# Optimization experiments

Hardware: AMD Instinct MI355X
Metric: run time of the kernel (lower is better)

The kernel has to match this reference:

```python
import jax, jax.numpy as jnp
import numpy as np

H = 512
N = 512
BSZ = 8
L = 4096
DIRECTION = 2  # 0=forward, 1=backward, 2=bidirectional (split N in half)


def setup_inputs() -> dict:
    key = jax.random.key(0)
    k = jax.random.split(key, 6)
    u = jax.random.normal(k[0], (BSZ, L, H), jnp.float32)
    # variable lengths in [L//2, L]
    lengths = jax.random.randint(k[1], (BSZ,), L // 2, L + 1).astype(jnp.int32)
    # LRU init: r_min=0, r_max=1, max_phase=2*pi
    u1 = jax.random.uniform(k[2], (N,), jnp.float32)
    nu_log = jnp.log(-0.5 * jnp.log(u1))
    u2 = jax.random.uniform(k[3], (N,), jnp.float32)
    theta_log = jnp.log(2.0 * np.pi * u2)
    lam = jnp.exp(-jnp.exp(nu_log) + 1j * jnp.exp(theta_log))  # (N,) complex
    gamma = jnp.sqrt(1.0 - jnp.abs(lam) ** 2)[:, None]          # (N,1)
    B = jax.random.normal(k[4], (H, N, 2), jnp.float32) / np.float32(np.sqrt(2 * H)) * gamma
    C = jax.random.normal(k[5], (2, H, N), jnp.float32) / np.float32(np.sqrt(N))
    return {"u": u, "lengths": lengths, "nu_log": nu_log, "theta_log": theta_log, "B": B, "C": C}


def _lru_scan(lam, Bu, reverse):
    """Diagonal linear recurrence x_t = lam * x_{t-1} + Bu_t along axis 2 via associative scan.
    lam: (n,) complex; Bu: (B, n, L) complex."""
    a = jnp.broadcast_to(lam[None, :, None], Bu.shape)

    def op(e1, e2):
        a1, b1 = e1
        a2, b2 = e2
        return a1 * a2, a2 * b1 + b2

    _, x = jax.lax.associative_scan(op, (a, Bu), axis=2, reverse=reverse)
    return x


def reference(u, lengths, nu_log, theta_log, B, C):
    lam = jnp.exp(-jnp.exp(nu_log) + 1j * jnp.exp(theta_log))  # (N,)
    Bc = B[..., 0] + 1j * B[..., 1]                            # (H, N) complex
    Bu = jnp.einsum('blh,hn->bnl', u, Bc)                      # (B, N, L) complex
    mask = jnp.arange(L)[None, :] < lengths[:, None]           # (B, L)
    Bu = Bu * mask[:, None, :]
    if DIRECTION == 2:
        h = N // 2
        x = jnp.concatenate([
            _lru_scan(lam[:h], Bu[:, :h], reverse=False),
            _lru_scan(lam[h:], Bu[:, h:], reverse=True),
        ], axis=1)
    elif DIRECTION == 0:
        x = _lru_scan(lam, Bu, reverse=False)
    else:
        x = _lru_scan(lam, Bu, reverse=True)
    x = x * mask[:, None, :]           # zero outputs past each sequence length
    x = jnp.swapaxes(x, 1, 2)          # (B, L, N)
    y = x.real @ C[0] - x.imag @ C[1]  # (B, L, H)  (requires H == N, as in source)
    return y
```

## Files before the change

kernel.cpp:

```cpp
#include <hip/hip_runtime.h>

#define L_SEQ   4096
#define BSZQ    8
#define ROWS    (BSZQ * L_SEQ)
#define KC1     512
#define NC1     1024
#define KC2     1024
#define NC2     512
#define CHUNK   64
#define NCHUNK  64

typedef __attribute__((ext_vector_type(8))) short bfrag;
typedef __attribute__((ext_vector_type(4))) float ffrag;

static __device__ __forceinline__ unsigned short f2bf(float f) {
    union { float f; unsigned int u; } v; v.f = f;
    unsigned int r = v.u + 0x7fffu + ((v.u >> 16) & 1u);
    return (unsigned short)(r >> 16);
}
static __device__ __forceinline__ unsigned int pk2(float a, float b) {
    return (unsigned int)f2bf(a) | ((unsigned int)f2bf(b) << 16);
}
static __device__ __forceinline__ float2 unpk2(unsigned int u) {
    union { unsigned int u; float f; } a, b;
    a.u = u << 16;
    b.u = u & 0xffff0000u;
    return make_float2(a.f, b.f);
}

static __device__ __forceinline__ void async16(const void* g, void* l) {
    __builtin_amdgcn_global_load_lds(
        (const __attribute__((address_space(1))) unsigned int*)g,
        (__attribute__((address_space(3))) unsigned int*)l,
        16, 0, 0);
}

__global__ __launch_bounds__(256) void prep_all_kernel(
    const float* __restrict__ B, const float* __restrict__ C,
    const float* __restrict__ nu_log, const float* __restrict__ theta_log,
    unsigned short* __restrict__ Bt, unsigned short* __restrict__ Dt,
    float2* __restrict__ lam)
{
    int g = blockIdx.x, tid = threadIdx.x;
    if (g < 2048) {
        int idx = g * 256 + tid;
        int n2 = idx >> 9, h = idx & 511;
        Bt[idx] = f2bf(B[(size_t)h * 1024 + n2]);
    } else if (g < 4096) {
        int idx = (g - 2048) * 256 + tid;
        int j = idx >> 10, k = idx & 1023;
        int n = k >> 1, c = k & 1;
        float v = C[((size_t)c * 512 + n) * 512 + j];
        Dt[idx] = f2bf(c ? -v : v);
    } else {
#pragma unroll
        for (int r = 0; r < 2; r++) {
            int n = tid + r * 256;
            float mag = expf(-expf(nu_log[n]));
            float th  = expf(theta_log[n]);
            lam[n] = make_float2(mag * cosf(th), mag * sinf(th));
        }
    }
}

__global__ __launch_bounds__(256) void conv_mask_kernel(
    const float* __restrict__ u, const int* __restrict__ lengths,
    unsigned short* __restrict__ ub)
{
    int idx = blockIdx.x * 256 + threadIdx.x;
    int row = idx >> 6;
    int l = row & (L_SEQ - 1), b = row >> 12;
    bool keep = (l < lengths[b]);
    union { unsigned int s[4]; float4 f; } o;
    if (keep) {
        const float4 a = *(const float4*)(u + (size_t)idx * 8);
        const float4 c = *(const float4*)(u + (size_t)idx * 8 + 4);
        o.s[0] = pk2(a.x, a.y); o.s[1] = pk2(a.z, a.w);
        o.s[2] = pk2(c.x, c.y); o.s[3] = pk2(c.z, c.w);
    } else {
        o.s[0] = o.s[1] = o.s[2] = o.s[3] = 0u;
    }
    *(float4*)(ub + (size_t)idx * 8) = o.f;
}

template<int KD, int ND, bool BF16OUT>
__global__ __launch_bounds__(256, 4) void gemm_db(
    const unsigned short* __restrict__ A,
    const unsigned short* __restrict__ Bt,
    void* __restrict__ Co)
{
    __shared__ __align__(16) unsigned short As[2][128 * 32];
    __shared__ __align__(16) unsigned short Bs[2][128 * 32];

    const int tid  = threadIdx.x;
    const int lane = tid & 63, w = tid >> 6;
    const int q = lane >> 4, m16 = lane & 15;
    const int wr = (w >> 1) * 64, wc = (w & 1) * 64;
    const int row0 = blockIdx.x * 128;
    const int col0 = blockIdx.y * 128;

    ffrag acc[4][4];
#pragma unroll
    for (int i = 0; i < 4; i++)
#pragma unroll
        for (int j = 0; j < 4; j++) acc[i][j] = (ffrag)0.f;

#define STAGE_T(GP, TB, KT, GR0) do {                                          \
    _Pragma("unroll")                                                          \
    for (int j_ = 0; j_ < 2; j_++) {                                           \
        int s_ = j_ * 256 + tid;                                               \
        int r_ = s_ >> 2;                                                      \
        int cs_ = (s_ & 3) ^ ((r_ >> 1) & 3);                                  \
        async16(GP + (size_t)((GR0) + r_) * KD + (KT) + cs_ * 8,               \
                &TB[(size_t)(j_ * 256 + w * 64) * 8]);                         \
    }                                                                          \
} while (0)

    STAGE_T(A,  As[0], 0, row0);
    STAGE_T(Bt, Bs[0], 0, col0);
    __syncthreads();

    int c = 0;
    for (int kt = 0; kt < KD; kt += 32) {
        if (kt + 32 < KD) {
            STAGE_T(A,  As[c ^ 1], kt + 32, row0);
            STAGE_T(Bt, Bs[c ^ 1], kt + 32, col0);
        }
        bfrag a[4], b[4];
#pragma unroll
        for (int ri = 0; ri < 4; ri++) {
            int r_ = wr + ri * 16 + m16;
            a[ri] = *(const bfrag*)&As[c][r_ * 32 + (q ^ ((r_ >> 1) & 3)) * 8];
        }
#pragma unroll
        for (int ci = 0; ci < 4; ci++) {
            int r_ = wc + ci * 16 + m16;
            b[ci] = *(const bfrag*)&Bs[c][r_ * 32 + (q ^ ((r_ >> 1) & 3)) * 8];
        }
#pragma unroll
        for (int ri = 0; ri < 4; ri++)
#pragma unroll
            for (int ci = 0; ci < 4; ci++)
                acc[ri][ci] = __builtin_amdgcn_mfma_f32_16x16x32_bf16(
                    a[ri], b[ci], acc[ri][ci], 0, 0, 0);
        __syncthreads();
        c ^= 1;
    }
#undef STAGE_T

    if (BF16OUT) {
        unsigned int* Cb = (unsigned int*)Co;
        const int colc0 = (col0 >> 1) + (w & 1) * 32;
#pragma unroll
        for (int ri = 0; ri < 4; ri++)
#pragma unroll
            for (int cp = 0; cp < 2; cp++)
#pragma unroll
                for (int r4 = 0; r4 < 4; r4++) {
                    float a0 = acc[ri][cp * 2][r4];
                    float a1 = acc[ri][cp * 2 + 1][r4];
                    float b0 = __shfl_xor(a0, 1);
                    float b1 = __shfl_xor(a1, 1);
                    unsigned int uo = (m16 & 1) ? pk2(b1, a1) : pk2(a0, b0);
                    int row = row0 + wr + ri * 16 + q * 4 + r4;
                    int ccol = (cp * 2 + (m16 & 1)) * 8 + (m16 >> 1);
                    Cb[(size_t)row * (ND / 2) + colc0 + ccol] = uo;
                }
    } else {
        float* Cf = (float*)Co;
#pragma unroll
        for (int ri = 0; ri < 4; ri++)
#pragma unroll
            for (int r4 = 0; r4 < 4; r4++) {
                int row = row0 + wr + ri * 16 + q * 4 + r4;
#pragma unroll
                for (int ci = 0; ci < 4; ci++) {
                    int col = col0 + wc + ci * 16 + m16;
                    Cf[(size_t)row * ND + col] = acc[ri][ci][r4];
                }
            }
    }
}

__global__ __launch_bounds__(512) void scan_states_kernel(
    const unsigned int* __restrict__ bu, const float2* __restrict__ lam,
    float2* __restrict__ states)
{
    int n = threadIdx.x;
    int b = blockIdx.x >> 6;
    int c = blockIdx.x & 63;
    float2 lm = lam[n];
    float xr = 0.f, xi = 0.f;
    bool fwd = (n < 256);
    int l0 = fwd ? (c * CHUNK) : (c * CHUNK + CHUNK - 1);
    const unsigned int* p = bu + ((size_t)b * L_SEQ + l0) * 512 + n;
    ptrdiff_t step = fwd ? 512 : -512;
#pragma unroll 8
    for (int t = 0; t < CHUNK; t++) {
        float2 v = unpk2(*p);
        float nr = lm.x * xr - lm.y * xi + v.x;
        float ni = lm.x * xi + lm.y * xr + v.y;
        xr = nr; xi = ni;
        p += step;
    }
    states[((size_t)b * NCHUNK + c) * 512 + n] = make_float2(xr, xi);
}

__global__ __launch_bounds__(512) void scan_combine_kernel(
    const float2* __restrict__ states, float2* __restrict__ carries,
    const float2* __restrict__ lam)
{
    int n = threadIdx.x;
    int b = blockIdx.x;
    float2 lm = lam[n];
    float ar = lm.x, ai = lm.y;
#pragma unroll
    for (int i = 0; i < 6; i++) {
        float nr = ar * ar - ai * ai;
        ai = 2.f * ar * ai;
        ar = nr;
    }
    float cr = 0.f, ci = 0.f;
    bool fwd = (n < 256);
    for (int g = 0; g < 8; g++) {
        float2 s[8];
#pragma unroll
        for (int k = 0; k < 8; k++) {
            int c = fwd ? (g * 8 + k) : (63 - (g * 8 + k));
            s[k] = states[((size_t)b * NCHUNK + c) * 512 + n];
        }
#pragma unroll
        for (int k = 0; k < 8; k++) {
            int c = fwd ? (g * 8 + k) : (63 - (g * 8 + k));
            carries[((size_t)b * NCHUNK + c) * 512 + n] = make_float2(cr, ci);
            float nr = ar * cr - ai * ci + s[k].x;
            float ni = ar * ci + ai * cr + s[k].y;
            cr = nr; ci = ni;
        }
    }
}

__global__ __launch_bounds__(512) void scan_apply_kernel(
    unsigned int* __restrict__ bu, const float2* __restrict__ carries,
    const float2* __restrict__ lam, const int* __restrict__ lengths)
{
    int n = threadIdx.x;
    int b = blockIdx.x >> 6;
    int c = blockIdx.x & 63;
    int len = lengths[b];
    float2 lm = lam[n];
    float2 cy = carries[((size_t)b * NCHUNK + c) * 512 + n];
    bool fwd = (n < 256);
    int l0 = fwd ? (c * CHUNK) : (c * CHUNK + CHUNK - 1);
    int dl = fwd ? 1 : -1;
    unsigned int* p = bu + ((size_t)b * L_SEQ + l0) * 512 + n;
    ptrdiff_t step = fwd ? 512 : -512;
    float xr = cy.x, xi = cy.y;
    int l = l0;
#pragma unroll 8
    for (int t = 0; t < CHUNK; t++) {
        float2 v = unpk2(*p);
        float nr = lm.x * xr - lm.y * xi + v.x;
        float ni = lm.x * xi + lm.y * xr + v.y;
        xr = nr; xi = ni;
        *p = (l >= len) ? 0u : pk2(xr, xi);
        p += step; l += dl;
    }
}

extern "C" void kernel_launch(void* const* d_in, const int* in_sizes, int n_in,
                              void* d_out, int out_size, void* d_ws, size_t ws_size,
                              hipStream_t stream)
{
    const float* u        = (const float*)d_in[0];
    const int*   lengths  = (const int*)  d_in[1];
    const float* nu_log   = (const float*)d_in[2];
    const float* theta_log= (const float*)d_in[3];
    const float* B        = (const float*)d_in[4];
    const float* C        = (const float*)d_in[5];
    float* y = (float*)d_out;

    char* wp = (char*)d_ws;
    float2* lam     = (float2*)wp;  wp += 4096;
    float2* states  = (float2*)wp;  wp += (size_t)BSZQ * NCHUNK * 512 * 8;
    float2* carries = (float2*)wp;  wp += (size_t)BSZQ * NCHUNK * 512 * 8;
    unsigned int* bu = (unsigned int*)wp; wp += (size_t)ROWS * 512 * 4;
    unsigned short* ub = (unsigned short*)wp; wp += (size_t)ROWS * 512 * 2;
    unsigned short* Bt = (unsigned short*)wp; wp += (size_t)NC1 * KC1 * 2;
    unsigned short* Dt = (unsigned short*)wp; wp += (size_t)NC2 * KC2 * 2;

    prep_all_kernel<<<4097, 256, 0, stream>>>(B, C, nu_log, theta_log, Bt, Dt, lam);
    conv_mask_kernel<<<8192, 256, 0, stream>>>(u, lengths, ub);

    {
        dim3 grid(ROWS / 128, NC1 / 128);
        gemm_db<KC1, NC1, true><<<grid, 256, 0, stream>>>(ub, Bt, bu);
    }

    scan_states_kernel<<<BSZQ * NCHUNK, 512, 0, stream>>>(bu, lam, states);
    scan_combine_kernel<<<BSZQ, 512, 0, stream>>>(states, carries, lam);
    scan_apply_kernel<<<BSZQ * NCHUNK, 512, 0, stream>>>(bu, carries, lam, lengths);

    {
        dim3 grid(ROWS / 128, NC2 / 128);
        gemm_db<KC2, NC2, false><<<grid, 256, 0, stream>>>(
            (const unsigned short*)bu, Dt, y);
    }
}
```

Baseline: 272.1 us.

## Triple-buffer GEMM LDS staging with vmcnt waits and XCD-aware block remap

Replaces the double-buffered GEMM with a three-stage LDS ring that keeps two tiles in flight and uses explicit vmcnt waits plus one barrier per iteration instead of two syncthreads. It also flattens the grid to 1D and remaps block IDs so consecutive tiles land on the same XCD (blockIdx mod 8), improving L2 reuse of A/B panels. The costs are extra LDS per block, with occupancy hints dropping from 4 to 3 blocks per CU, and a dependence on exact async-load counts for correctness.

```diff
diff --git a/kernel.cpp b/kernel.cpp
--- a/kernel.cpp
+++ b/kernel.cpp
@@ -84,20 +84,25 @@
 }
 
 template<int KD, int ND, bool BF16OUT>
-__global__ __launch_bounds__(256, 4) void gemm_db(
+__global__ __launch_bounds__(256, 3) void gemm_tb(
     const unsigned short* __restrict__ A,
     const unsigned short* __restrict__ Bt,
     void* __restrict__ Co)
 {
-    __shared__ __align__(16) unsigned short As[2][128 * 32];
-    __shared__ __align__(16) unsigned short Bs[2][128 * 32];
+    __shared__ __align__(16) unsigned short As[3][128 * 32];
+    __shared__ __align__(16) unsigned short Bs[3][128 * 32];
 
     const int tid  = threadIdx.x;
     const int lane = tid & 63, w = tid >> 6;
     const int q = lane >> 4, m16 = lane & 15;
     const int wr = (w >> 1) * 64, wc = (w & 1) * 64;
-    const int row0 = blockIdx.x * 128;
-    const int col0 = blockIdx.y * 128;
+
+    constexpr int GY = ND / 128;
+    const int nwg = gridDim.x;
+    const int Q = nwg >> 3;
+    const int o = (blockIdx.x & 7) * Q + (blockIdx.x >> 3);
+    const int row0 = (o / GY) * 128;
+    const int col0 = (o & (GY - 1)) * 128;
 
     ffrag acc[4][4];
 #pragma unroll
@@ -116,15 +121,21 @@
     }                                                                          \
 } while (0)
 
-    STAGE_T(A,  As[0], 0, row0);
-    STAGE_T(Bt, Bs[0], 0, col0);
-    __syncthreads();
-
-    int c = 0;
-    for (int kt = 0; kt < KD; kt += 32) {
-        if (kt + 32 < KD) {
-            STAGE_T(A,  As[c ^ 1], kt + 32, row0);
-            STAGE_T(Bt, Bs[c ^ 1], kt + 32, col0);
+    STAGE_T(A,  As[0], 0,  row0);
+    STAGE_T(Bt, Bs[0], 0,  col0);
+    STAGE_T(A,  As[1], 32, row0);
+    STAGE_T(Bt, Bs[1], 32, col0);
+
+    constexpr int NT = KD / 32;
+    int c = 0, cs = 2;
+    for (int i = 0; i < NT; ++i) {
+        if (i + 1 < NT) asm volatile("s_waitcnt vmcnt(4)" ::: "memory");
+        else            asm volatile("s_waitcnt vmcnt(0)" ::: "memory");
+        __builtin_amdgcn_s_barrier();
+        __builtin_amdgcn_sched_barrier(0);
+        if (i + 2 < NT) {
+            STAGE_T(A,  As[cs], (i + 2) * 32, row0);
+            STAGE_T(Bt, Bs[cs], (i + 2) * 32, col0);
         }
         bfrag a[4], b[4];
 #pragma unroll
@@ -143,8 +154,8 @@
             for (int ci = 0; ci < 4; ci++)
                 acc[ri][ci] = __builtin_amdgcn_mfma_f32_16x16x32_bf16(
                     a[ri], b[ci], acc[ri][ci], 0, 0, 0);
-        __syncthreads();
-        c ^= 1;
+        c  = (c  + 1 == 3) ? 0 : c  + 1;
+        cs = (cs + 1 == 3) ? 0 : cs + 1;
     }
 #undef STAGE_T
 
@@ -292,18 +303,13 @@
     prep_all_kernel<<<4097, 256, 0, stream>>>(B, C, nu_log, theta_log, Bt, Dt, lam);
     conv_mask_kernel<<<8192, 256, 0, stream>>>(u, lengths, ub);
 
-    {
-        dim3 grid(ROWS / 128, NC1 / 128);
-        gemm_db<KC1, NC1, true><<<grid, 256, 0, stream>>>(ub, Bt, bu);
-    }
+    gemm_tb<KC1, NC1, true><<<(ROWS / 128) * (NC1 / 128), 256, 0, stream>>>(
+        ub, Bt, bu);
 
     scan_states_kernel<<<BSZQ * NCHUNK, 512, 0, stream>>>(bu, lam, states);
     scan_combine_kernel<<<BSZQ, 512, 0, stream>>>(states, carries, lam);
     scan_apply_kernel<<<BSZQ * NCHUNK, 512, 0, stream>>>(bu, carries, lam, lengths);
 
-    {
-        dim3 grid(ROWS / 128, NC2 / 128);
-        gemm_db<KC2, NC2, false><<<grid, 256, 0, stream>>>(
-            (const unsigned short*)bu, Dt, y);
-    }
-}
+    gemm_tb<KC2, NC2, false><<<(ROWS / 128) * (NC2 / 128), 256, 0, stream>>>(
+        (const unsigned short*)bu, Dt, y);
+}
```

Result: no change. 273.6 us (+0.6%).

## Fuse fp32-to-bf16 conversion and masking into first GEMM, vectorize scans, remap tiles

Applied to the files above, without the earlier changes.

Drops the separate conversion/mask kernel. The first GEMM now loads fp32 input rows straight from global memory into registers, packs them to bf16, applies the length mask and writes them to swizzled shared memory, which avoids the round trip through a bf16 intermediate buffer. Both GEMMs use a 1D grid with a block remapping that interleaves tiles, likely for cache locality. The scan kernels now have each thread handle two adjacent state channels with 64-bit loads and stores. The cost is that A-tile loads become synchronous register loads instead of async copies, which may expose latency in the GEMM mainloop.

```diff
diff --git a/kernel.cpp b/kernel.cpp
--- a/kernel.cpp
+++ b/kernel.cpp
@@ -63,31 +63,11 @@
     }
 }
 
-__global__ __launch_bounds__(256) void conv_mask_kernel(
-    const float* __restrict__ u, const int* __restrict__ lengths,
-    unsigned short* __restrict__ ub)
-{
-    int idx = blockIdx.x * 256 + threadIdx.x;
-    int row = idx >> 6;
-    int l = row & (L_SEQ - 1), b = row >> 12;
-    bool keep = (l < lengths[b]);
-    union { unsigned int s[4]; float4 f; } o;
-    if (keep) {
-        const float4 a = *(const float4*)(u + (size_t)idx * 8);
-        const float4 c = *(const float4*)(u + (size_t)idx * 8 + 4);
-        o.s[0] = pk2(a.x, a.y); o.s[1] = pk2(a.z, a.w);
-        o.s[2] = pk2(c.x, c.y); o.s[3] = pk2(c.z, c.w);
-    } else {
-        o.s[0] = o.s[1] = o.s[2] = o.s[3] = 0u;
-    }
-    *(float4*)(ub + (size_t)idx * 8) = o.f;
-}
-
-template<int KD, int ND, bool BF16OUT>
-__global__ __launch_bounds__(256, 4) void gemm_db(
-    const unsigned short* __restrict__ A,
+__global__ __launch_bounds__(256, 4) void gemm1_conv(
+    const float* __restrict__ U,
     const unsigned short* __restrict__ Bt,
-    void* __restrict__ Co)
+    const int* __restrict__ lengths,
+    unsigned int* __restrict__ Cb)
 {
     __shared__ __align__(16) unsigned short As[2][128 * 32];
     __shared__ __align__(16) unsigned short Bs[2][128 * 32];
@@ -96,8 +76,17 @@
     const int lane = tid & 63, w = tid >> 6;
     const int q = lane >> 4, m16 = lane & 15;
     const int wr = (w >> 1) * 64, wc = (w & 1) * 64;
-    const int row0 = blockIdx.x * 128;
-    const int col0 = blockIdx.y * 128;
+
+    const int o = (blockIdx.x & 7) * 256 + (blockIdx.x >> 3);
+    const int row0 = (o >> 3) * 128;
+    const int col0 = (o & 7) * 128;
+
+    const int ar = tid >> 1;
+    const int ah = tid & 1;
+    const int as_ = (ar >> 1) & 3;
+    const int grow = row0 + ar;
+    const bool keep = (grow & (L_SEQ - 1)) < lengths[grow >> 12];
+    const float* pA = U + (size_t)grow * KC1 + ah * 16;
 
     ffrag acc[4][4];
 #pragma unroll
@@ -105,26 +94,130 @@
 #pragma unroll
         for (int j = 0; j < 4; j++) acc[i][j] = (ffrag)0.f;
 
-#define STAGE_T(GP, TB, KT, GR0) do {                                          \
+    float4 fa[4];
+
+#define LOADA(KT) do {                                                         \
+    _Pragma("unroll")                                                          \
+    for (int i_ = 0; i_ < 4; i_++)                                             \
+        fa[i_] = *(const float4*)(pA + (KT) + i_ * 4);                         \
+} while (0)
+
+#define CWRITE(BUF) do {                                                       \
+    uint4 lo_ = make_uint4(pk2(fa[0].x, fa[0].y), pk2(fa[0].z, fa[0].w),       \
+                           pk2(fa[1].x, fa[1].y), pk2(fa[1].z, fa[1].w));      \
+    uint4 hi_ = make_uint4(pk2(fa[2].x, fa[2].y), pk2(fa[2].z, fa[2].w),       \
+                           pk2(fa[3].x, fa[3].y), pk2(fa[3].z, fa[3].w));      \
+    if (!keep) { lo_ = make_uint4(0u,0u,0u,0u); hi_ = make_uint4(0u,0u,0u,0u); } \
+    *(uint4*)&BUF[ar * 32 + ((2 * ah)     ^ as_) * 8] = lo_;                   \
+    *(uint4*)&BUF[ar * 32 + ((2 * ah + 1) ^ as_) * 8] = hi_;                   \
+} while (0)
+
+#define STAGE_B1(TB, KT) do {                                                  \
     _Pragma("unroll")                                                          \
     for (int j_ = 0; j_ < 2; j_++) {                                           \
         int s_ = j_ * 256 + tid;                                               \
         int r_ = s_ >> 2;                                                      \
         int cs_ = (s_ & 3) ^ ((r_ >> 1) & 3);                                  \
-        async16(GP + (size_t)((GR0) + r_) * KD + (KT) + cs_ * 8,               \
+        async16(Bt + (size_t)(col0 + r_) * KC1 + (KT) + cs_ * 8,               \
                 &TB[(size_t)(j_ * 256 + w * 64) * 8]);                         \
     }                                                                          \
 } while (0)
 
-    STAGE_T(A,  As[0], 0, row0);
-    STAGE_T(Bt, Bs[0], 0, col0);
+    LOADA(0);
+    STAGE_B1(Bs[0], 0);
+    CWRITE(As[0]);
     __syncthreads();
 
     int c = 0;
-    for (int kt = 0; kt < KD; kt += 32) {
-        if (kt + 32 < KD) {
-            STAGE_T(A,  As[c ^ 1], kt + 32, row0);
-            STAGE_T(Bt, Bs[c ^ 1], kt + 32, col0);
+    for (int kt = 0; kt < KC1; kt += 32) {
+        const bool nl = (kt + 32 < KC1);
+        if (nl) { LOADA(kt + 32); STAGE_B1(Bs[c ^ 1], kt + 32); }
+        bfrag a[4], b[4];
+#pragma unroll
+        for (int ri = 0; ri < 4; ri++) {
+            int r_ = wr + ri * 16 + m16;
+            a[ri] = *(const bfrag*)&As[c][r_ * 32 + (q ^ ((r_ >> 1) & 3)) * 8];
+        }
+#pragma unroll
+        for (int ci = 0; ci < 4; ci++) {
+            int r_ = wc + ci * 16 + m16;
+            b[ci] = *(const bfrag*)&Bs[c][r_ * 32 + (q ^ ((r_ >> 1) & 3)) * 8];
+        }
+#pragma unroll
+        for (int ri = 0; ri < 4; ri++)
+#pragma unroll
+            for (int ci = 0; ci < 4; ci++)
+                acc[ri][ci] = __builtin_amdgcn_mfma_f32_16x16x32_bf16(
+                    a[ri], b[ci], acc[ri][ci], 0, 0, 0);
+        if (nl) CWRITE(As[c ^ 1]);
+        __syncthreads();
+        c ^= 1;
+    }
+#undef LOADA
+#undef CWRITE
+#undef STAGE_B1
+
+    const int colc0 = (col0 >> 1) + (w & 1) * 32;
+#pragma unroll
+    for (int ri = 0; ri < 4; ri++)
+#pragma unroll
+        for (int cp = 0; cp < 2; cp++)
+#pragma unroll
+            for (int r4 = 0; r4 < 4; r4++) {
+                float a0 = acc[ri][cp * 2][r4];
+                float a1 = acc[ri][cp * 2 + 1][r4];
+                float b0 = __shfl_xor(a0, 1);
+                float b1 = __shfl_xor(a1, 1);
+                unsigned int uo = (m16 & 1) ? pk2(b1, a1) : pk2(a0, b0);
+                int row = row0 + wr + ri * 16 + q * 4 + r4;
+                int ccol = (cp * 2 + (m16 & 1)) * 8 + (m16 >> 1);
+                Cb[(size_t)row * (NC1 / 2) + colc0 + ccol] = uo;
+            }
+}
+
+__global__ __launch_bounds__(256, 4) void gemm2_db(
+    const unsigned short* __restrict__ A,
+    const unsigned short* __restrict__ Bt,
+    float* __restrict__ Cf)
+{
+    __shared__ __align__(16) unsigned short As[2][128 * 32];
+    __shared__ __align__(16) unsigned short Bs[2][128 * 32];
+
+    const int tid  = threadIdx.x;
+    const int lane = tid & 63, w = tid >> 6;
+    const int q = lane >> 4, m16 = lane & 15;
+    const int wr = (w >> 1) * 64, wc = (w & 1) * 64;
+
+    const int o = (blockIdx.x & 7) * 128 + (blockIdx.x >> 3);
+    const int row0 = (o >> 2) * 128;
+    const int col0 = (o & 3) * 128;
+
+    ffrag acc[4][4];
+#pragma unroll
+    for (int i = 0; i < 4; i++)
+#pragma unroll
+        for (int j = 0; j < 4; j++) acc[i][j] = (ffrag)0.f;
+
+#define STAGE_T2(GP, TB, KT, GR0) do {                                         \
+    _Pragma("unroll")                                                          \
+    for (int j_ = 0; j_ < 2; j_++) {                                           \
+        int s_ = j_ * 256 + tid;                                               \
+        int r_ = s_ >> 2;                                                      \
+        int cs_ = (s_ & 3) ^ ((r_ >> 1) & 3);                                  \
+        async16(GP + (size_t)((GR0) + r_) * KC2 + (KT) + cs_ * 8,              \
+                &TB[(size_t)(j_ * 256 + w * 64) * 8]);                         \
+    }                                                                          \
+} while (0)
+
+    STAGE_T2(A,  As[0], 0, row0);
+    STAGE_T2(Bt, Bs[0], 0, col0);
+    __syncthreads();
+
+    int c = 0;
+    for (int kt = 0; kt < KC2; kt += 32) {
+        if (kt + 32 < KC2) {
+            STAGE_T2(A,  As[c ^ 1], kt + 32, row0);
+            STAGE_T2(Bt, Bs[c ^ 1], kt + 32, col0);
         }
         bfrag a[4], b[4];
 #pragma unroll
@@ -146,64 +239,47 @@
         __syncthreads();
         c ^= 1;
     }
-#undef STAGE_T
-
-    if (BF16OUT) {
-        unsigned int* Cb = (unsigned int*)Co;
-        const int colc0 = (col0 >> 1) + (w & 1) * 32;
-#pragma unroll
-        for (int ri = 0; ri < 4; ri++)
-#pragma unroll
-            for (int cp = 0; cp < 2; cp++)
-#pragma unroll
-                for (int r4 = 0; r4 < 4; r4++) {
-                    float a0 = acc[ri][cp * 2][r4];
-                    float a1 = acc[ri][cp * 2 + 1][r4];
-                    float b0 = __shfl_xor(a0, 1);
-                    float b1 = __shfl_xor(a1, 1);
-                    unsigned int uo = (m16 & 1) ? pk2(b1, a1) : pk2(a0, b0);
-                    int row = row0 + wr + ri * 16 + q * 4 + r4;
-                    int ccol = (cp * 2 + (m16 & 1)) * 8 + (m16 >> 1);
-                    Cb[(size_t)row * (ND / 2) + colc0 + ccol] = uo;
-                }
-    } else {
-        float* Cf = (float*)Co;
-#pragma unroll
-        for (int ri = 0; ri < 4; ri++)
-#pragma unroll
-            for (int r4 = 0; r4 < 4; r4++) {
-                int row = row0 + wr + ri * 16 + q * 4 + r4;
-#pragma unroll
-                for (int ci = 0; ci < 4; ci++) {
-                    int col = col0 + wc + ci * 16 + m16;
-                    Cf[(size_t)row * ND + col] = acc[ri][ci][r4];
-                }
+#undef STAGE_T2
+
+#pragma unroll
+    for (int ri = 0; ri < 4; ri++)
+#pragma unroll
+        for (int r4 = 0; r4 < 4; r4++) {
+            int row = row0 + wr + ri * 16 + q * 4 + r4;
+#pragma unroll
+            for (int ci = 0; ci < 4; ci++) {
+                int col = col0 + wc + ci * 16 + m16;
+                Cf[(size_t)row * NC2 + col] = acc[ri][ci][r4];
             }
-    }
-}
-
-__global__ __launch_bounds__(512) void scan_states_kernel(
+        }
+}
+
+__global__ __launch_bounds__(256) void scan_states_kernel(
     const unsigned int* __restrict__ bu, const float2* __restrict__ lam,
     float2* __restrict__ states)
 {
-    int n = threadIdx.x;
+    int t = threadIdx.x;
     int b = blockIdx.x >> 6;
     int c = blockIdx.x & 63;
-    float2 lm = lam[n];
-    float xr = 0.f, xi = 0.f;
-    bool fwd = (n < 256);
+    float4 lm = *(const float4*)&lam[2 * t];
+    float x0r = 0.f, x0i = 0.f, x1r = 0.f, x1i = 0.f;
+    bool fwd = (t < 128);
     int l0 = fwd ? (c * CHUNK) : (c * CHUNK + CHUNK - 1);
-    const unsigned int* p = bu + ((size_t)b * L_SEQ + l0) * 512 + n;
+    const unsigned int* p = bu + ((size_t)b * L_SEQ + l0) * 512 + 2 * t;
     ptrdiff_t step = fwd ? 512 : -512;
 #pragma unroll 8
-    for (int t = 0; t < CHUNK; t++) {
-        float2 v = unpk2(*p);
-        float nr = lm.x * xr - lm.y * xi + v.x;
-        float ni = lm.x * xi + lm.y * xr + v.y;
-        xr = nr; xi = ni;
+    for (int i = 0; i < CHUNK; i++) {
+        uint2 v = *(const uint2*)p;
+        float2 v0 = unpk2(v.x), v1 = unpk2(v.y);
+        float n0r = lm.x * x0r - lm.y * x0i + v0.x;
+        float n0i = lm.x * x0i + lm.y * x0r + v0.y;
+        float n1r = lm.z * x1r - lm.w * x1i + v1.x;
+        float n1i = lm.z * x1i + lm.w * x1r + v1.y;
+        x0r = n0r; x0i = n0i; x1r = n1r; x1i = n1i;
         p += step;
     }
-    states[((size_t)b * NCHUNK + c) * 512 + n] = make_float2(xr, xi);
+    *(float4*)&states[((size_t)b * NCHUNK + c) * 512 + 2 * t] =
+        make_float4(x0r, x0i, x1r, x1i);
 }
 
 __global__ __launch_bounds__(512) void scan_combine_kernel(
@@ -240,30 +316,36 @@
     }
 }
 
-__global__ __launch_bounds__(512) void scan_apply_kernel(
+__global__ __launch_bounds__(256) void scan_apply_kernel(
     unsigned int* __restrict__ bu, const float2* __restrict__ carries,
     const float2* __restrict__ lam, const int* __restrict__ lengths)
 {
-    int n = threadIdx.x;
+    int t = threadIdx.x;
     int b = blockIdx.x >> 6;
     int c = blockIdx.x & 63;
     int len = lengths[b];
-    float2 lm = lam[n];
-    float2 cy = carries[((size_t)b * NCHUNK + c) * 512 + n];
-    bool fwd = (n < 256);
+    float4 lm = *(const float4*)&lam[2 * t];
+    float4 cy = *(const float4*)&carries[((size_t)b * NCHUNK + c) * 512 + 2 * t];
+    bool fwd = (t < 128);
     int l0 = fwd ? (c * CHUNK) : (c * CHUNK + CHUNK - 1);
     int dl = fwd ? 1 : -1;
-    unsigned int* p = bu + ((size_t)b * L_SEQ + l0) * 512 + n;
+    unsigned int* p = bu + ((size_t)b * L_SEQ + l0) * 512 + 2 * t;
     ptrdiff_t step = fwd ? 512 : -512;
-    float xr = cy.x, xi = cy.y;
+    float x0r = cy.x, x0i = cy.y, x1r = cy.z, x1i = cy.w;
     int l = l0;
 #pragma unroll 8
-    for (int t = 0; t < CHUNK; t++) {
-        float2 v = unpk2(*p);
-        float nr = lm.x * xr - lm.y * xi + v.x;
-        float ni = lm.x * xi + lm.y * xr + v.y;
-        xr = nr; xi = ni;
-        *p = (l >= len) ? 0u : pk2(xr, xi);
+    for (int i = 0; i < CHUNK; i++) {
+        uint2 v = *(const uint2*)p;
+        float2 v0 = unpk2(v.x), v1 = unpk2(v.y);
+        float n0r = lm.x * x0r - lm.y * x0i + v0.x;
+        float n0i = lm.x * x0i + lm.y * x0r + v0.y;
+        float n1r = lm.z * x1r - lm.w * x1i + v1.x;
+        float n1i = lm.z * x1i + lm.w * x1r + v1.y;
+        x0r = n0r; x0i = n0i; x1r = n1r; x1i = n1i;
+        uint2 o2;
+        o2.x = (l >= len) ? 0u : pk2(x0r, x0i);
+        o2.y = (l >= len) ? 0u : pk2(x1r, x1i);
+        *(uint2*)p = o2;
         p += step; l += dl;
     }
 }
@@ -285,25 +367,18 @@
     float2* states  = (float2*)wp;  wp += (size_t)BSZQ * NCHUNK * 512 * 8;
     float2* carries = (float2*)wp;  wp += (size_t)BSZQ * NCHUNK * 512 * 8;
     unsigned int* bu = (unsigned int*)wp; wp += (size_t)ROWS * 512 * 4;
-    unsigned short* ub = (unsigned short*)wp; wp += (size_t)ROWS * 512 * 2;
     unsigned short* Bt = (unsigned short*)wp; wp += (size_t)NC1 * KC1 * 2;
     unsigned short* Dt = (unsigned short*)wp; wp += (size_t)NC2 * KC2 * 2;
 
     prep_all_kernel<<<4097, 256, 0, stream>>>(B, C, nu_log, theta_log, Bt, Dt, lam);
-    conv_mask_kernel<<<8192, 256, 0, stream>>>(u, lengths, ub);
-
-    {
-        dim3 grid(ROWS / 128, NC1 / 128);
-        gemm_db<KC1, NC1, true><<<grid, 256, 0, stream>>>(ub, Bt, bu);
-    }
-
-    scan_states_kernel<<<BSZQ * NCHUNK, 512, 0, stream>>>(bu, lam, states);
+
+    gemm1_conv<<<(ROWS / 128) * (NC1 / 128), 256, 0, stream>>>(
+        u, Bt, lengths, bu);
+
+    scan_states_kernel<<<BSZQ * NCHUNK, 256, 0, stream>>>(bu, lam, states);
     scan_combine_kernel<<<BSZQ, 512, 0, stream>>>(states, carries, lam);
-    scan_apply_kernel<<<BSZQ * NCHUNK, 512, 0, stream>>>(bu, carries, lam, lengths);
-
-    {
-        dim3 grid(ROWS / 128, NC2 / 128);
-        gemm_db<KC2, NC2, false><<<grid, 256, 0, stream>>>(
-            (const unsigned short*)bu, Dt, y);
-    }
-}
+    scan_apply_kernel<<<BSZQ * NCHUNK, 256, 0, stream>>>(bu, carries, lam, lengths);
+
+    gemm2_db<<<(ROWS / 128) * (NC2 / 128), 256, 0, stream>>>(
+        (const unsigned short*)bu, Dt, y);
+}
```

New measurement: 292.5 us. 7.5% more time.

## Fuse scan carry combine into apply kernel and process two channels per thread

Applied to the files above, without the earlier changes.

Removes the separate single-block-per-batch carry combine kernel. Each apply block now recomputes its own carry by serially folding the preceding chunk states. Both scan kernels also handle two complex channels per thread with 8-byte loads and stores, halving the thread count. This drops a low-parallelism launch and the carries buffer, at the cost of redundant state reads and combine arithmetic in every block.

```diff
diff --git a/kernel.cpp b/kernel.cpp
--- a/kernel.cpp
+++ b/kernel.cpp
@@ -182,88 +182,93 @@
     }
 }
 
-__global__ __launch_bounds__(512) void scan_states_kernel(
+__global__ __launch_bounds__(256) void scan_states_kernel(
     const unsigned int* __restrict__ bu, const float2* __restrict__ lam,
     float2* __restrict__ states)
 {
-    int n = threadIdx.x;
+    int t = threadIdx.x;
     int b = blockIdx.x >> 6;
     int c = blockIdx.x & 63;
-    float2 lm = lam[n];
-    float xr = 0.f, xi = 0.f;
-    bool fwd = (n < 256);
+    float4 lm = *(const float4*)&lam[2 * t];
+    float x0r = 0.f, x0i = 0.f, x1r = 0.f, x1i = 0.f;
+    bool fwd = (t < 128);
     int l0 = fwd ? (c * CHUNK) : (c * CHUNK + CHUNK - 1);
-    const unsigned int* p = bu + ((size_t)b * L_SEQ + l0) * 512 + n;
+    const unsigned int* p = bu + ((size_t)b * L_SEQ + l0) * 512 + 2 * t;
     ptrdiff_t step = fwd ? 512 : -512;
 #pragma unroll 8
-    for (int t = 0; t < CHUNK; t++) {
-        float2 v = unpk2(*p);
-        float nr = lm.x * xr - lm.y * xi + v.x;
-        float ni = lm.x * xi + lm.y * xr + v.y;
-        xr = nr; xi = ni;
+    for (int i = 0; i < CHUNK; i++) {
+        uint2 v = *(const uint2*)p;
+        float2 v0 = unpk2(v.x), v1 = unpk2(v.y);
+        float n0r = lm.x * x0r - lm.y * x0i + v0.x;
+        float n0i = lm.x * x0i + lm.y * x0r + v0.y;
+        float n1r = lm.z * x1r - lm.w * x1i + v1.x;
+        float n1i = lm.z * x1i + lm.w * x1r + v1.y;
+        x0r = n0r; x0i = n0i; x1r = n1r; x1i = n1i;
         p += step;
     }
-    states[((size_t)b * NCHUNK + c) * 512 + n] = make_float2(xr, xi);
-}
-
-__global__ __launch_bounds__(512) void scan_combine_kernel(
-    const float2* __restrict__ states, float2* __restrict__ carries,
-    const float2* __restrict__ lam)
-{
-    int n = threadIdx.x;
-    int b = blockIdx.x;
-    float2 lm = lam[n];
-    float ar = lm.x, ai = lm.y;
-#pragma unroll
-    for (int i = 0; i < 6; i++) {
-        float nr = ar * ar - ai * ai;
-        ai = 2.f * ar * ai;
-        ar = nr;
-    }
-    float cr = 0.f, ci = 0.f;
-    bool fwd = (n < 256);
-    for (int g = 0; g < 8; g++) {
-        float2 s[8];
-#pragma unroll
-        for (int k = 0; k < 8; k++) {
-            int c = fwd ? (g * 8 + k) : (63 - (g * 8 + k));
-            s[k] = states[((size_t)b * NCHUNK + c) * 512 + n];
-        }
-#pragma unroll
-        for (int k = 0; k < 8; k++) {
-            int c = fwd ? (g * 8 + k) : (63 - (g * 8 + k));
-            carries[((size_t)b * NCHUNK + c) * 512 + n] = make_float2(cr, ci);
-            float nr = ar * cr - ai * ci + s[k].x;
-            float ni = ar * ci + ai * cr + s[k].y;
-            cr = nr; ci = ni;
-        }
-    }
-}
-
-__global__ __launch_bounds__(512) void scan_apply_kernel(
-    unsigned int* __restrict__ bu, const float2* __restrict__ carries,
+    *(float4*)&states[((size_t)b * NCHUNK + c) * 512 + 2 * t] =
+        make_float4(x0r, x0i, x1r, x1i);
+}
+
+__global__ __launch_bounds__(256) void scan_fix_apply_kernel(
+    unsigned int* __restrict__ bu, const float2* __restrict__ states,
     const float2* __restrict__ lam, const int* __restrict__ lengths)
 {
-    int n = threadIdx.x;
+    int t = threadIdx.x;
     int b = blockIdx.x >> 6;
     int c = blockIdx.x & 63;
     int len = lengths[b];
-    float2 lm = lam[n];
-    float2 cy = carries[((size_t)b * NCHUNK + c) * 512 + n];
-    bool fwd = (n < 256);
+    bool fwd = (t < 128);
+    float4 lm = *(const float4*)&lam[2 * t];
+
+    float a0r = lm.x, a0i = lm.y, a1r = lm.z, a1i = lm.w;
+#pragma unroll
+    for (int i = 0; i < 6; i++) {
+        float n0r = a0r * a0r - a0i * a0i; a0i = 2.f * a0r * a0i; a0r = n0r;
+        float n1r = a1r * a1r - a1i * a1i; a1i = 2.f * a1r * a1i; a1r = n1r;
+    }
+
+    float c0r = 0.f, c0i = 0.f, c1r = 0.f, c1i = 0.f;
+    for (int g = 0; g < 8; ++g) {
+        float4 s[8];
+#pragma unroll
+        for (int k = 0; k < 8; ++k) {
+            int cc = fwd ? (g * 8 + k) : (63 - (g * 8 + k));
+            s[k] = *(const float4*)&states[((size_t)b * NCHUNK + cc) * 512 + 2 * t];
+        }
+#pragma unroll
+        for (int k = 0; k < 8; ++k) {
+            int cc = fwd ? (g * 8 + k) : (63 - (g * 8 + k));
+            bool use = fwd ? (cc < c) : (cc > c);
+            if (use) {
+                float n0r = a0r * c0r - a0i * c0i + s[k].x;
+                float n0i = a0r * c0i + a0i * c0r + s[k].y;
+                float n1r = a1r * c1r - a1i * c1i + s[k].z;
+                float n1i = a1r * c1i + a1i * c1r + s[k].w;
+                c0r = n0r; c0i = n0i; c1r = n1r; c1i = n1i;
+            }
+        }
+    }
+
     int l0 = fwd ? (c * CHUNK) : (c * CHUNK + CHUNK - 1);
     int dl = fwd ? 1 : -1;
-    unsigned int* p = bu + ((size_t)b * L_SEQ + l0) * 512 + n;
+    unsigned int* p = bu + ((size_t)b * L_SEQ + l0) * 512 + 2 * t;
     ptrdiff_t step = fwd ? 512 : -512;
-    float xr = cy.x, xi = cy.y;
+    float x0r = c0r, x0i = c0i, x1r = c1r, x1i = c1i;
     int l = l0;
 #pragma unroll 8
-    for (int t = 0; t < CHUNK; t++) {
-        float2 v = unpk2(*p);
-        float nr = lm.x * xr - lm.y * xi + v.x;
-        float ni = lm.x * xi + lm.y * xr + v.y;
-        xr = nr; xi = ni;
-        *p = (l >= len) ? 0u : pk2(xr, xi);
+    for (int i = 0; i < CHUNK; i++) {
+        uint2 v = *(const uint2*)p;
+        float2 v0 = unpk2(v.x), v1 = unpk2(v.y);
+        float n0r = lm.x * x0r - lm.y * x0i + v0.x;
+        float n0i = lm.x * x0i + lm.y * x0r + v0.y;
+        float n1r = lm.z * x1r - lm.w * x1i + v1.x;
+        float n1i = lm.z * x1i + lm.w * x1r + v1.y;
+        x0r = n0r; x0i = n0i; x1r = n1r; x1i = n1i;
+        uint2 o2;
+        o2.x = (l >= len) ? 0u : pk2(x0r, x0i);
+        o2.y = (l >= len) ? 0u : pk2(x1r, x1i);
+        *(uint2*)p = o2;
         p += step; l += dl;
     }
 }
@@ -283,7 +288,6 @@
     char* wp = (char*)d_ws;
     float2* lam     = (float2*)wp;  wp += 4096;
     float2* states  = (float2*)wp;  wp += (size_t)BSZQ * NCHUNK * 512 * 8;
-    float2* carries = (float2*)wp;  wp += (size_t)BSZQ * NCHUNK * 512 * 8;
     unsigned int* bu = (unsigned int*)wp; wp += (size_t)ROWS * 512 * 4;
     unsigned short* ub = (unsigned short*)wp; wp += (size_t)ROWS * 512 * 2;
     unsigned short* Bt = (unsigned short*)wp; wp += (size_t)NC1 * KC1 * 2;
@@ -297,9 +301,8 @@
         gemm_db<KC1, NC1, true><<<grid, 256, 0, stream>>>(ub, Bt, bu);
     }
 
-    scan_states_kernel<<<BSZQ * NCHUNK, 512, 0, stream>>>(bu, lam, states);
-    scan_combine_kernel<<<BSZQ, 512, 0, stream>>>(states, carries, lam);
-    scan_apply_kernel<<<BSZQ * NCHUNK, 512, 0, stream>>>(bu, carries, lam, lengths);
+    scan_states_kernel<<<BSZQ * NCHUNK, 256, 0, stream>>>(bu, lam, states);
+    scan_fix_apply_kernel<<<BSZQ * NCHUNK, 256, 0, stream>>>(bu, states, lam, lengths);
 
     {
         dim3 grid(ROWS / 128, NC2 / 128);
```

Result: no change. 273.6 us (+0.5%).
